# Optimization experiments

Measured on AMD Instinct MI355X. Metric: run time of the kernel, lower is better.

The kernel has to match this reference:

```python
import jax, jax.numpy as jnp
import numpy as np

B, C, N = 16, 128, 2048  # batch, channels (SA_Layer(128)), num points


def setup_inputs() -> dict:
    key = jax.random.key(0)
    ks = jax.random.split(key, 6)
    x = jax.random.normal(ks[0], (B, C, N), jnp.float32)
    wq = jax.random.normal(ks[1], (C // 4, C), jnp.float32) * 0.05  # shared q/k 1x1 conv, no bias
    wv = jax.random.normal(ks[2], (C, C), jnp.float32) * 0.05
    bv = jax.random.normal(ks[3], (C,), jnp.float32) * 0.05
    wt = jax.random.normal(ks[4], (C, C), jnp.float32) * 0.05
    bt = jax.random.normal(ks[5], (C,), jnp.float32) * 0.05
    gamma = jnp.ones((C,), jnp.float32)   # BatchNorm1d weight
    beta = jnp.zeros((C,), jnp.float32)   # BatchNorm1d bias
    bn_mean = jnp.zeros((C,), jnp.float32)  # running mean (eval mode)
    bn_var = jnp.ones((C,), jnp.float32)    # running var (eval mode)
    return dict(x=x, wq=wq, wv=wv, bv=bv, wt=wt, bt=bt,
                gamma=gamma, beta=beta, bn_mean=bn_mean, bn_var=bn_var)


def reference(x, wq, wv, bv, wt, bt, gamma, beta, bn_mean, bn_var):
    EPS = 1e-9
    BN_EPS = 1e-5
    # q_conv and k_conv share weights (tied in __init__)
    x_q = jnp.einsum('dc,bcn->bnd', wq, x)               # [B, N, C/4]
    x_k = jnp.einsum('dc,bcn->bdn', wq, x)               # [B, C/4, N]
    energy = jnp.einsum('bnd,bdm->bnm', x_q, x_k)        # [B, N, N]
    attn = jax.nn.softmax(energy, axis=-1)
    # offset-attention renormalization: divide by column sum
    attn = attn / (EPS + attn.sum(axis=1, keepdims=True))
    x_v = jnp.einsum('dc,bcn->bdn', wv, x) + bv[None, :, None]   # [B, C, N]
    x_r = jnp.einsum('bdn,bnm->bdm', x_v, attn)                  # [B, C, N]
    t = jnp.einsum('dc,bcn->bdn', wt, x - x_r) + bt[None, :, None]
    # BatchNorm1d (eval mode) + ReLU
    t = (t - bn_mean[None, :, None]) * jax.lax.rsqrt(bn_var + BN_EPS)[None, :, None]
    t = t * gamma[None, :, None] + beta[None, :, None]
    return x + jax.nn.relu(t)
```

## Files before the change

### kernel.cpp

```cpp
#include <hip/hip_runtime.h>
#include <hip/hip_bf16.h>
#include <math.h>

#define BB 16
#define CC 128
#define NN 2048
#define CQ 32

typedef __attribute__((ext_vector_type(8))) short bf16x8;
typedef __attribute__((ext_vector_type(4))) float f32x4;
typedef __attribute__((ext_vector_type(16))) float f32x16;
typedef unsigned char uchar;

__device__ __forceinline__ ushort f2b(float f) {
    __hip_bfloat16 h = __float2bfloat16(f);
    return *reinterpret_cast<ushort*>(&h);
}
__device__ __forceinline__ float b2f(ushort u) {
    union { unsigned u; float f; } v; v.u = ((unsigned)u) << 16;
    return v.f;
}
__device__ __forceinline__ uint f2q4(float a, float b, float c, float d) {
    int r = __builtin_amdgcn_cvt_pk_fp8_f32(a, b, 0, false);
    r = __builtin_amdgcn_cvt_pk_fp8_f32(c, d, r, true);
    return (uint)r;
}
__device__ __forceinline__ bf16x8 as_b8(uint4 u) {
    union { uint4 u; bf16x8 b; } v; v.u = u; return v.b;
}
__device__ __forceinline__ bf16x8 as_b8_2(uint2 a, uint2 b) {
    return as_b8(make_uint4(a.x, a.y, b.x, b.y));
}
__device__ __forceinline__ float fexp2(float x) {
    return __builtin_amdgcn_exp2f(x);
}
union U2L { uint2 u; long l; };

#define OFF_VB  524288
#define OFF_RSI 4718592

#define QSCALE 1.2011224087864498f

__global__ __launch_bounds__(512) void k_proj(const float* __restrict__ x,
        const float* __restrict__ wq, const float* __restrict__ wv,
        const float* __restrict__ bv, ushort* __restrict__ Qt, uchar* __restrict__ Vb) {
    __shared__ ushort Wl[160][136];
    __shared__ ushort Xs[128][136];
    int bid = (blockIdx.x & 7) * 32 + (blockIdx.x >> 3);
    int b  = bid >> 4;
    int n0 = (bid & 15) << 7;
    int tid = threadIdx.x;
    #pragma unroll
    for (int k = 0; k < 10; ++k) {
        int idx = k * 512 + tid;
        int r = idx >> 5, c4 = (idx & 31) << 2;
        const float* srcw = (r < 32) ? (wq + r * 128 + c4) : (wv + (r - 32) * 128 + c4);
        float4 w4 = *(const float4*)srcw;
        float s = (r < 32) ? QSCALE : 1.0f;
        *(ushort4*)&Wl[r][c4] = make_ushort4(f2b(w4.x * s), f2b(w4.y * s),
                                             f2b(w4.z * s), f2b(w4.w * s));
    }
    const float* xb = x + (size_t)b * CC * NN;
    for (int idx = tid; idx < 4096; idx += 512) {
        int c = idx >> 5, n4 = (idx & 31) << 2;
        float4 xv = *(const float4*)&xb[c * NN + n0 + n4];
        Xs[n4][c]     = f2b(xv.x);
        Xs[n4 + 1][c] = f2b(xv.y);
        Xs[n4 + 2][c] = f2b(xv.z);
        Xs[n4 + 3][c] = f2b(xv.w);
    }
    __syncthreads();
    int w = tid >> 6, l = tid & 63, lr = l & 15, lg = l >> 4;
    f32x4 zero = {0.f, 0.f, 0.f, 0.f};
    int nn = n0 + w * 16 + lr;
    for (int dt = 0; dt < 10; ++dt) {
        f32x4 acc = zero;
        #pragma unroll
        for (int k = 0; k < 4; ++k) {
            bf16x8 a  = *(const bf16x8*)&Wl[dt * 16 + lr][k * 32 + lg * 8];
            bf16x8 bx = *(const bf16x8*)&Xs[w * 16 + lr][k * 32 + lg * 8];
            acc = __builtin_amdgcn_mfma_f32_16x16x32_bf16(a, bx, acc, 0, 0, 0);
        }
        if (dt < 2) {
            ushort4 p = make_ushort4(f2b(acc[0]), f2b(acc[1]), f2b(acc[2]), f2b(acc[3]));
            *(ushort4*)&Qt[(size_t)(b * NN + nn) * CQ + dt * 16 + lg * 4] = p;
        } else {
            union { uint u; uchar c[4]; } q;
            int vd = (dt - 2) * 16 + lg * 4;
            q.u = f2q4(acc[0] + bv[vd], acc[1] + bv[vd + 1],
                       acc[2] + bv[vd + 2], acc[3] + bv[vd + 3]);
            #pragma unroll
            for (int i = 0; i < 4; ++i)
                Vb[(size_t)(b * CC + vd + i) * NN + nn] = q.c[i];
        }
    }
}

__global__ __launch_bounds__(512) void k_rowstats(const ushort* __restrict__ Qt,
        float* __restrict__ RSI) {
    __shared__ ushort Qm[2][128][36];
    __shared__ float Sred[2][64];
    int bid = (blockIdx.x & 7) * 64 + (blockIdx.x >> 3);
    int b  = bid >> 5;
    int n0 = (bid & 31) << 6;
    int tid = threadIdx.x;
    int w = tid >> 6, l = tid & 63, lr = l & 15, lg = l >> 4;
    int wn = w & 3, wm = w >> 2;
    const ushort* Qtb = Qt + (size_t)b * NN * CQ;
    bf16x8 aq = *(const bf16x8*)&Qtb[(size_t)(n0 + wn * 16 + lr) * CQ + lg * 8];
    int sr = tid >> 2, sc = (tid & 3) * 8;
    *(uint4*)&Qm[0][sr][sc] = *(const uint4*)&Qtb[(size_t)sr * CQ + sc];
    float S[4] = {0.f, 0.f, 0.f, 0.f};
    f32x4 zero = {0.f, 0.f, 0.f, 0.f};
    __syncthreads();
    for (int t = 0; t < 16; ++t) {
        int cur = t & 1;
        uint4 q0;
        if (t < 15)
            q0 = *(const uint4*)&Qtb[(size_t)((t + 1) * 128 + sr) * CQ + sc];
        #pragma unroll
        for (int mi = 0; mi < 4; ++mi) {
            bf16x8 bq = *(const bf16x8*)&Qm[cur][(wm * 4 + mi) * 16 + lr][lg * 8];
            f32x4 e = __builtin_amdgcn_mfma_f32_16x16x32_bf16(aq, bq, zero, 0, 0, 0);
            S[0] += fexp2(e[0]); S[1] += fexp2(e[1]);
            S[2] += fexp2(e[2]); S[3] += fexp2(e[3]);
        }
        if (t < 15)
            *(uint4*)&Qm[cur ^ 1][sr][sc] = q0;
        __syncthreads();
    }
    #pragma unroll
    for (int d = 1; d < 16; d <<= 1) {
        #pragma unroll
        for (int i = 0; i < 4; ++i) S[i] += __shfl_xor(S[i], d);
    }
    if (lr == 0) {
        #pragma unroll
        for (int i = 0; i < 4; ++i) Sred[wm][wn * 16 + lg * 4 + i] = S[i];
    }
    __syncthreads();
    if (tid < 64)
        RSI[b * NN + n0 + tid] = 256.f / (Sred[0][tid] + Sred[1][tid]);
}

__global__ __launch_bounds__(1024, 4) void k_attn_pv(const ushort* __restrict__ Qt,
        const uchar* __restrict__ Vb, const float* __restrict__ RSI,
        const float* __restrict__ x, const float* __restrict__ wt,
        const float* __restrict__ bt, const float* __restrict__ gamma,
        const float* __restrict__ beta, const float* __restrict__ bn_mean,
        const float* __restrict__ bn_var, float* __restrict__ out) {
    __shared__ uchar SMp[2][2][128][72];
    __shared__ ushort wtl[16896];
    __shared__ float csred[4][128];
    __shared__ float csum[128];
    __shared__ float fAl[128], fBl[128];
    int bid = (blockIdx.x & 7) * 32 + (blockIdx.x >> 3);
    int b  = bid >> 4;
    int m0 = (bid & 15) << 7;
    int tid = threadIdx.x;
    int w = tid >> 6, l = tid & 63, lr = l & 15, lg = l >> 4;
    const ushort* Qtb = Qt + (size_t)b * NN * CQ;
    const uchar*  Vbb = Vb + (size_t)b * CC * NN;
    const float*  RSb = RSI + (size_t)b * NN;
    const float*  xb  = x   + (size_t)b * CC * NN;
    float*        outb = out + (size_t)b * CC * NN;
    f32x4 zero = {0.f, 0.f, 0.f, 0.f};
    bool producer = (w < 8);

    for (int idx = tid; idx < 4096; idx += 1024) {
        int r = idx >> 5, c4 = (idx & 31) << 2;
        float4 w4 = *(const float4*)&wt[r * 128 + c4];
        *(ushort4*)&wtl[r * 132 + c4] =
            make_ushort4(f2b(w4.x), f2b(w4.y), f2b(w4.z), f2b(w4.w));
    }
    if (tid < 128) {
        float A = gamma[tid] * rsqrtf(bn_var[tid] + 1e-5f);
        fAl[tid] = A;
        fBl[tid] = (bt[tid] - bn_mean[tid]) * A + beta[tid];
    }

    int wn = w & 3, mh = w >> 2;
    bf16x8 bm[4];
    float cs[4] = {0.f, 0.f, 0.f, 0.f};
    int sv = 0, shv = 0;
    const uchar* vsrc = nullptr;
    bf16x8 aq_nx; float4 rsi_nx;
    int cw = w - 8;
    int dq = cw >> 1, mh2 = cw & 1;
    int ar = l & 31, kh = l >> 5;
    f32x16 pacc0, pacc1;

    if (producer) {
        #pragma unroll
        for (int mi = 0; mi < 4; ++mi)
            bm[mi] = *(const bf16x8*)&Qtb[(size_t)(m0 + (mh * 4 + mi) * 16 + lr) * CQ + lg * 8];
        sv = tid >> 2; shv = (tid & 3) * 16;
        vsrc = Vbb + (size_t)sv * NN + shv;
        {
            uint4 v0 = *(const uint4*)(vsrc);
            uchar* dst = &SMp[0][0][sv][shv];
            *(uint2*)(dst)     = make_uint2(v0.x, v0.y);
            *(uint2*)(dst + 8) = make_uint2(v0.z, v0.w);
        }
        {
            bf16x8 aq0 = *(const bf16x8*)&Qtb[(size_t)(wn * 16 + lr) * CQ + lg * 8];
            float4 r4 = *(const float4*)&RSb[wn * 16 + lg * 4];
            int nb = wn * 16 + lg * 4;
            #pragma unroll
            for (int mi = 0; mi < 4; ++mi) {
                f32x4 e = __builtin_amdgcn_mfma_f32_16x16x32_bf16(aq0, bm[mi], zero, 0, 0, 0);
                float w0 = fexp2(e[0]) * r4.x;
                float w1 = fexp2(e[1]) * r4.y;
                float w2 = fexp2(e[2]) * r4.z;
                float w3 = fexp2(e[3]) * r4.w;
                cs[mi] += w0 + w1 + w2 + w3;
                *(uint*)&SMp[1][0][(mh * 4 + mi) * 16 + lr][nb] = f2q4(w0, w1, w2, w3);
            }
        }
        aq_nx  = *(const bf16x8*)&Qtb[(size_t)(64 + wn * 16 + lr) * CQ + lg * 8];
        rsi_nx = *(const float4*)&RSb[64 + wn * 16 + lg * 4];
    } else {
        #pragma unroll
        for (int r = 0; r < 16; ++r) { pacc0[r] = 0.f; pacc1[r] = 0.f; }
    }
    __syncthreads();
    for (int t = 0; t < 32; ++t) {
        int cur = t & 1;
        if (producer) {
            if (t < 31) {
                int ntn = (t + 1) * 64;
                uint4 v0 = *(const uint4*)(vsrc + ntn);
                bf16x8 aq = aq_nx;
                float4 r4 = rsi_nx;
                if (t < 30) {
                    int nt2 = (t + 2) * 64;
                    aq_nx  = *(const bf16x8*)&Qtb[(size_t)(nt2 + wn * 16 + lr) * CQ + lg * 8];
                    rsi_nx = *(const float4*)&RSb[nt2 + wn * 16 + lg * 4];
                }
                int nb = wn * 16 + lg * 4;
                #pragma unroll
                for (int mi = 0; mi < 4; ++mi) {
                    f32x4 e = __builtin_amdgcn_mfma_f32_16x16x32_bf16(aq, bm[mi], zero, 0, 0, 0);
                    float w0 = fexp2(e[0]) * r4.x;
                    float w1 = fexp2(e[1]) * r4.y;
                    float w2 = fexp2(e[2]) * r4.z;
                    float w3 = fexp2(e[3]) * r4.w;
                    cs[mi] += w0 + w1 + w2 + w3;
                    *(uint*)&SMp[1][cur ^ 1][(mh * 4 + mi) * 16 + lr][nb] =
                        f2q4(w0, w1, w2, w3);
                }
                uchar* dst = &SMp[0][cur ^ 1][sv][shv];
                *(uint2*)(dst)     = make_uint2(v0.x, v0.y);
                *(uint2*)(dst + 8) = make_uint2(v0.z, v0.w);
            }
        } else {
            __builtin_amdgcn_s_setprio(1);
            #pragma unroll
            for (int kk = 0; kk < 4; ++kk) {
                int cb = kk * 16 + kh * 8;
                U2L va, wb0, wb1;
                va.u  = *(const uint2*)&SMp[0][cur][dq * 32 + ar][cb];
                wb0.u = *(const uint2*)&SMp[1][cur][mh2 * 64 + ar][cb];
                wb1.u = *(const uint2*)&SMp[1][cur][mh2 * 64 + 32 + ar][cb];
                pacc0 = __builtin_amdgcn_mfma_f32_32x32x16_fp8_fp8(va.l, wb0.l, pacc0, 0, 0, 0);
                pacc1 = __builtin_amdgcn_mfma_f32_32x32x16_fp8_fp8(va.l, wb1.l, pacc1, 0, 0, 0);
            }
            __builtin_amdgcn_s_setprio(0);
        }
        __syncthreads();
    }
    if (producer) {
        #pragma unroll
        for (int mi = 0; mi < 4; ++mi) {
            cs[mi] += __shfl_xor(cs[mi], 16);
            cs[mi] += __shfl_xor(cs[mi], 32);
        }
        if (lg == 0) {
            #pragma unroll
            for (int mi = 0; mi < 4; ++mi)
                csred[wn][(mh * 4 + mi) * 16 + lr] = cs[mi];
        }
    }
    __syncthreads();
    if (tid < 128) {
        float tot = csred[0][tid] + csred[1][tid] + csred[2][tid] + csred[3][tid];
        csum[tid] = 1.f / (2.56e-7f + tot);
    }
    __syncthreads();
    ushort* UsP = (ushort*)&SMp[0][0][0][0];
    if (!producer) {
        float inv0 = csum[mh2 * 64 + ar];
        float inv1 = csum[mh2 * 64 + 32 + ar];
        int mA = m0 + mh2 * 64 + ar;
        int mL = mh2 * 64 + ar;
        #pragma unroll
        for (int g = 0; g < 4; ++g) {
            int db = dq * 32 + 8 * g + 4 * kh;
            ushort4 u0, u1;
            #pragma unroll
            for (int j = 0; j < 4; ++j) {
                int r = 4 * g + j;
                float x0 = xb[(size_t)(db + j) * NN + mA];
                float x1 = xb[(size_t)(db + j) * NN + mA + 32];
                ((ushort*)&u0)[j] = f2b(x0 - pacc0[r] * inv0);
                ((ushort*)&u1)[j] = f2b(x1 - pacc1[r] * inv1);
            }
            *(ushort4*)&UsP[mL * 132 + db]        = u0;
            *(ushort4*)&UsP[(mL + 32) * 132 + db] = u1;
        }
    }
    __syncthreads();
    {
        int tile = w;
        int rt = tile >> 2, mt = tile & 3;
        f32x16 acc;
        #pragma unroll
        for (int r = 0; r < 16; ++r) acc[r] = 0.f;
        #pragma unroll
        for (int kk = 0; kk < 8; ++kk) {
            const ushort* ap = &wtl[(rt * 32 + ar) * 132 + kk * 16 + kh * 8];
            uint2 a0 = *(const uint2*)ap; uint2 a1 = *(const uint2*)(ap + 4);
            const ushort* bp = &UsP[(mt * 32 + ar) * 132 + kk * 16 + kh * 8];
            uint2 b0 = *(const uint2*)bp; uint2 b1 = *(const uint2*)(bp + 4);
            acc = __builtin_amdgcn_mfma_f32_32x32x16_bf16(
                as_b8_2(a0, a1), as_b8_2(b0, b1), acc, 0, 0, 0);
        }
        int m = m0 + mt * 32 + ar;
        #pragma unroll
        for (int g = 0; g < 4; ++g) {
            #pragma unroll
            for (int j = 0; j < 4; ++j) {
                int r = rt * 32 + j + 8 * g + 4 * kh;
                float t = acc[4 * g + j] * fAl[r] + fBl[r];
                t = fmaxf(t, 0.f);
                outb[(size_t)r * NN + m] = xb[(size_t)r * NN + m] + t;
            }
        }
    }
}

extern "C" void kernel_launch(void* const* d_in, const int* in_sizes, int n_in,
                              void* d_out, int out_size, void* d_ws, size_t ws_size,
                              hipStream_t stream) {
    const float* x       = (const float*)d_in[0];
    const float* wq      = (const float*)d_in[1];
    const float* wv      = (const float*)d_in[2];
    const float* bv      = (const float*)d_in[3];
    const float* wt      = (const float*)d_in[4];
    const float* bt      = (const float*)d_in[5];
    const float* gamma   = (const float*)d_in[6];
    const float* beta    = (const float*)d_in[7];
    const float* bn_mean = (const float*)d_in[8];
    const float* bn_var  = (const float*)d_in[9];
    float* out = (float*)d_out;
    float* ws  = (float*)d_ws;

    ushort* Qt   = (ushort*)ws;
    uchar*  Vbp  = (uchar*)(ws + OFF_VB);
    float*  RSI  = ws + OFF_RSI;

    k_proj<<<BB * 16, 512, 0, stream>>>(x, wq, wv, bv, Qt, Vbp);
    k_rowstats<<<BB * 32, 512, 0, stream>>>(Qt, RSI);
    k_attn_pv<<<BB * 16, 1024, 0, stream>>>(Qt, Vbp, RSI, x, wt, bt, gamma, beta,
                                            bn_mean, bn_var, out);
}
```

Measured before the change: 56.79 us.

## Fuse row-statistics pass into attention kernel via cooperative grid sync

Removes the separate row-stats kernel and computes the per-row softmax normalizers inside the attention kernel's prologue. Each block computes exp-sums for its 128 rows across all 2048 columns, using 16 waves that each cover 128 columns. It then writes the reciprocal to global memory and waits at a grid-wide barrier before the main loop. This saves one kernel launch and lets the stats work overlap with the weight and BN setup, at the cost of a cooperative launch and a grid.sync. It also requires all 256 blocks of 1024 threads to be co-resident.

New measurement: 86.08 us. 1.52x slower.

```diff
diff --git a/kernel.cpp b/kernel.cpp
--- a/kernel.cpp
+++ b/kernel.cpp
@@ -1,6 +1,9 @@
 #include <hip/hip_runtime.h>
 #include <hip/hip_bf16.h>
+#include <hip/hip_cooperative_groups.h>
 #include <math.h>
+
+namespace cg = cooperative_groups;
 
 #define BB 16
 #define CC 128
@@ -96,55 +99,8 @@
     }
 }
 
-__global__ __launch_bounds__(512) void k_rowstats(const ushort* __restrict__ Qt,
-        float* __restrict__ RSI) {
-    __shared__ ushort Qm[2][128][36];
-    __shared__ float Sred[2][64];
-    int bid = (blockIdx.x & 7) * 64 + (blockIdx.x >> 3);
-    int b  = bid >> 5;
-    int n0 = (bid & 31) << 6;
-    int tid = threadIdx.x;
-    int w = tid >> 6, l = tid & 63, lr = l & 15, lg = l >> 4;
-    int wn = w & 3, wm = w >> 2;
-    const ushort* Qtb = Qt + (size_t)b * NN * CQ;
-    bf16x8 aq = *(const bf16x8*)&Qtb[(size_t)(n0 + wn * 16 + lr) * CQ + lg * 8];
-    int sr = tid >> 2, sc = (tid & 3) * 8;
-    *(uint4*)&Qm[0][sr][sc] = *(const uint4*)&Qtb[(size_t)sr * CQ + sc];
-    float S[4] = {0.f, 0.f, 0.f, 0.f};
-    f32x4 zero = {0.f, 0.f, 0.f, 0.f};
-    __syncthreads();
-    for (int t = 0; t < 16; ++t) {
-        int cur = t & 1;
-        uint4 q0;
-        if (t < 15)
-            q0 = *(const uint4*)&Qtb[(size_t)((t + 1) * 128 + sr) * CQ + sc];
-        #pragma unroll
-        for (int mi = 0; mi < 4; ++mi) {
-            bf16x8 bq = *(const bf16x8*)&Qm[cur][(wm * 4 + mi) * 16 + lr][lg * 8];
-            f32x4 e = __builtin_amdgcn_mfma_f32_16x16x32_bf16(aq, bq, zero, 0, 0, 0);
-            S[0] += fexp2(e[0]); S[1] += fexp2(e[1]);
-            S[2] += fexp2(e[2]); S[3] += fexp2(e[3]);
-        }
-        if (t < 15)
-            *(uint4*)&Qm[cur ^ 1][sr][sc] = q0;
-        __syncthreads();
-    }
-    #pragma unroll
-    for (int d = 1; d < 16; d <<= 1) {
-        #pragma unroll
-        for (int i = 0; i < 4; ++i) S[i] += __shfl_xor(S[i], d);
-    }
-    if (lr == 0) {
-        #pragma unroll
-        for (int i = 0; i < 4; ++i) Sred[wm][wn * 16 + lg * 4 + i] = S[i];
-    }
-    __syncthreads();
-    if (tid < 64)
-        RSI[b * NN + n0 + tid] = 256.f / (Sred[0][tid] + Sred[1][tid]);
-}
-
 __global__ __launch_bounds__(1024, 4) void k_attn_pv(const ushort* __restrict__ Qt,
-        const uchar* __restrict__ Vb, const float* __restrict__ RSI,
+        const uchar* __restrict__ Vb, float* __restrict__ RSI,
         const float* __restrict__ x, const float* __restrict__ wt,
         const float* __restrict__ bt, const float* __restrict__ gamma,
         const float* __restrict__ beta, const float* __restrict__ bn_mean,
@@ -154,6 +110,7 @@
     __shared__ float csred[4][128];
     __shared__ float csum[128];
     __shared__ float fAl[128], fBl[128];
+    cg::grid_group grid = cg::this_grid();
     int bid = (blockIdx.x & 7) * 32 + (blockIdx.x >> 3);
     int b  = bid >> 4;
     int m0 = (bid & 15) << 7;
@@ -161,7 +118,7 @@
     int w = tid >> 6, l = tid & 63, lr = l & 15, lg = l >> 4;
     const ushort* Qtb = Qt + (size_t)b * NN * CQ;
     const uchar*  Vbb = Vb + (size_t)b * CC * NN;
-    const float*  RSb = RSI + (size_t)b * NN;
+    float*        RSb = RSI + (size_t)b * NN;
     const float*  xb  = x   + (size_t)b * CC * NN;
     float*        outb = out + (size_t)b * CC * NN;
     f32x4 zero = {0.f, 0.f, 0.f, 0.f};
@@ -177,6 +134,43 @@
         float A = gamma[tid] * rsqrtf(bn_var[tid] + 1e-5f);
         fAl[tid] = A;
         fBl[tid] = (bt[tid] - bn_mean[tid]) * A + beta[tid];
+    }
+
+    {
+        bf16x8 bmA[8];
+        #pragma unroll
+        for (int mi = 0; mi < 8; ++mi)
+            bmA[mi] = *(const bf16x8*)&Qtb[(size_t)(m0 + mi * 16 + lr) * CQ + lg * 8];
+        float csA[8] = {0.f, 0.f, 0.f, 0.f, 0.f, 0.f, 0.f, 0.f};
+        int nbase = w * 128;
+        #pragma unroll
+        for (int s = 0; s < 8; ++s) {
+            bf16x8 aqA = *(const bf16x8*)&Qtb[(size_t)(nbase + s * 16 + lr) * CQ + lg * 8];
+            #pragma unroll
+            for (int mi = 0; mi < 8; ++mi) {
+                f32x4 e = __builtin_amdgcn_mfma_f32_16x16x32_bf16(aqA, bmA[mi], zero, 0, 0, 0);
+                csA[mi] += fexp2(e[0]) + fexp2(e[1]) + fexp2(e[2]) + fexp2(e[3]);
+            }
+        }
+        #pragma unroll
+        for (int mi = 0; mi < 8; ++mi) {
+            csA[mi] += __shfl_xor(csA[mi], 16);
+            csA[mi] += __shfl_xor(csA[mi], 32);
+        }
+        float* csredA = (float*)&SMp[0][0][0][0];
+        if (lg == 0) {
+            #pragma unroll
+            for (int mi = 0; mi < 8; ++mi)
+                csredA[w * 128 + mi * 16 + lr] = csA[mi];
+        }
+        __syncthreads();
+        if (tid < 128) {
+            float tot = 0.f;
+            #pragma unroll
+            for (int w2 = 0; w2 < 16; ++w2) tot += csredA[w2 * 128 + tid];
+            RSb[m0 + tid] = 256.f / tot;
+        }
+        grid.sync();
     }
 
     int wn = w & 3, mh = w >> 2;
@@ -360,7 +354,10 @@
     float*  RSI  = ws + OFF_RSI;
 
     k_proj<<<BB * 16, 512, 0, stream>>>(x, wq, wv, bv, Qt, Vbp);
-    k_rowstats<<<BB * 32, 512, 0, stream>>>(Qt, RSI);
-    k_attn_pv<<<BB * 16, 1024, 0, stream>>>(Qt, Vbp, RSI, x, wt, bt, gamma, beta,
-                                            bn_mean, bn_var, out);
-}
+
+    void* args[] = {(void*)&Qt, (void*)&Vbp, (void*)&RSI, (void*)&x, (void*)&wt,
+                    (void*)&bt, (void*)&gamma, (void*)&beta, (void*)&bn_mean,
+                    (void*)&bn_var, (void*)&out};
+    hipLaunchCooperativeKernel((void*)k_attn_pv, dim3(BB * 16), dim3(1024),
+                               args, 0, stream);
+}
```
